# Kernel optimization log

Hardware: AMD Instinct MI355X
Metric: run time of the kernel (lower is better)

Reference implementation:

```python
import jax, jax.numpy as jnp
import numpy as np

C_V, C_F, C_D = 10, 64, 16
COSTS = jnp.array([10.0, 5.0, 2.0], dtype=jnp.float32)  # bandwidth cost per granularity
PENALTY = 0.0  # no_transmission_utility_penalty


def setup_inputs() -> dict:
    key = jax.random.key(0)
    k1, k2 = jax.random.split(key)
    B, H, W = 4, 192, 192
    collab = jax.random.normal(k1, (B, C_V + C_F + C_D, H, W), dtype=jnp.float32)
    utility = jax.random.normal(k2, (B, H, W, 3), dtype=jnp.float32)
    return {"collab_bev_data_list": collab, "utility_map_list": utility,
            "bandwidth_budget": 200000}


def _selection_mechanism(utility, budget_per_sample):
    # utility: [B, H, W, G]; returns [B, H, W] float selected granularity (-1 = none)
    B, H, W, G = utility.shape
    best_u = jnp.max(utility, axis=3)                      # [B,H,W]
    best_g = jnp.argmax(utility, axis=3)                   # [B,H,W]
    N = B * H * W
    flat_u = best_u.reshape(N)
    flat_g = best_g.reshape(N)
    b_idx = jnp.repeat(jnp.arange(B, dtype=jnp.int32), H * W)
    valid = flat_u > PENALTY
    cost = COSTS[flat_g]                                   # [N]
    # sort candidates by utility, descending (stable, matching list.sort)
    order = jnp.argsort(-flat_u)
    v_s = valid[order]
    c_s = cost[order]
    b_s = b_idx[order]

    # greedy budget-constrained selection per sample (sequential knapsack)
    def step(usage, item):
        v, c, b = item
        ok = v & (usage[b] + c <= budget_per_sample)
        usage = usage.at[b].add(jnp.where(ok, c, jnp.float32(0)))
        return usage, ok

    _, sel_sorted = jax.lax.scan(step, jnp.zeros((B,), jnp.float32), (v_s, c_s, b_s))
    selected = jnp.zeros((N,), bool).at[order].set(sel_sorted)
    idx = jnp.where(selected, flat_g.astype(jnp.float32), jnp.float32(-1.0))
    return idx.reshape(B, H, W)


def _build_sparse_bev(sel_idx, vox, feat, det):
    m0 = (sel_idx == 0.0)[:, None, :, :]
    m1 = (sel_idx == 1.0)[:, None, :, :]
    m2 = (sel_idx == 2.0)[:, None, :, :]
    return jnp.concatenate([vox * m0, feat * m1, det * m2], axis=1)


def reference(collab_bev_data_list, utility_map_list, bandwidth_budget):
    cav_num = collab_bev_data_list.shape[0]
    budget_per_sample = jnp.float32(bandwidth_budget / cav_num)
    sel_idx = _selection_mechanism(utility_map_list, budget_per_sample)
    vox = collab_bev_data_list[:, :C_V]
    feat = collab_bev_data_list[:, C_V:C_V + C_F]
    det = collab_bev_data_list[:, C_V + C_F:C_V + C_F + C_D]
    sparse = _build_sparse_bev(sel_idx, vox, feat, det)
    return sparse, sel_idx
```

## Files before the change

kernel.cpp:

```cpp
#include <hip/hip_runtime.h>
#include <stdint.h>
#include <math.h>

#define B_    4
#define HW    36864
#define NPIX  147456
#define C_V   10
#define C_F   64
#define C_D   16
#define C_ALL 90
#define HBINS 32768
#define CAP   1536
#define INV   0xFFFFFFFFu

#define OFF_HIST 0u
#define OFF_KEY  524288u
#define OFF_G    1114112u
#define OFF_SELX 1261568u
#define OFF_HL   1409024u

__device__ __forceinline__ uint32_t costOf(uint32_t g) {
    return g == 0u ? 10u : (g == 1u ? 5u : 2u);
}

__device__ __forceinline__ uint32_t budgetInt(const int* bptr) {
    double bps = (double)bptr[0] / (double)B_;
    float f = (float)bps;
    return (uint32_t)floorf(f);
}

#define CE(x, y) { uint64_t _mn = (x) < (y) ? (x) : (y); \
                   uint64_t _mx = (x) < (y) ? (y) : (x); (x) = _mx; (y) = _mn; }

__global__ void k_zero(uint4* __restrict__ w4) {
    uint32_t i = blockIdx.x * blockDim.x + threadIdx.x;
    w4[i] = make_uint4(0u, 0u, 0u, 0u);
}

__global__ void k_prep(const float* __restrict__ util, uint4* __restrict__ key4,
                       uint32_t* __restrict__ g4, uint32_t* __restrict__ selx4,
                       uint32_t* __restrict__ hist) {
    int t = blockIdx.x * blockDim.x + threadIdx.x;
    if (t >= NPIX / 4) return;
    const float4* u4 = (const float4*)util + (size_t)t * 3;
    float4 a = u4[0], b4 = u4[1], c4 = u4[2];
    float u[4][3] = { {a.x, a.y, a.z}, {a.w, b4.x, b4.y},
                      {b4.z, b4.w, c4.x}, {c4.y, c4.z, c4.w} };
    uint32_t kk[4]; uint32_t gpack = 0;
    #pragma unroll
    for (int p = 0; p < 4; ++p) {
        float best = u[p][0]; uint32_t g = 0;
        if (u[p][1] > best) { best = u[p][1]; g = 1; }
        if (u[p][2] > best) { best = u[p][2]; g = 2; }
        kk[p] = (best > 0.0f) ? (__float_as_uint(best) | 0x80000000u) : 0u;
        gpack |= g << (8 * p);
    }
    key4[t] = make_uint4(kk[0], kk[1], kk[2], kk[3]);
    g4[t] = gpack;
    selx4[t] = 0u;
    int b = (t * 4) / HW;
    #pragma unroll
    for (int p = 0; p < 4; ++p)
        if (kk[p])
            atomicAdd(&hist[(size_t)b * HBINS + ((kk[p] >> 16) & 32767u)],
                      costOf((gpack >> (8 * p)) & 3u));
}

__global__ __launch_bounds__(1024) void k_sel(const uint32_t* __restrict__ key,
                                              const uint8_t* __restrict__ g,
                                              const uint32_t* __restrict__ hist,
                                              const int* __restrict__ budget_ptr,
                                              uint8_t* __restrict__ selx,
                                              uint32_t* __restrict__ hl_out) {
    int b = blockIdx.x;
    int t = threadIdx.x;
    int lane = t & 63, wv = t >> 6;
    uint32_t budget = budgetInt(budget_ptr);
    const uint32_t* hb = hist + (size_t)b * HBINS;

    __shared__ uint32_t wsum[16];
    __shared__ uint32_t sh_b2, sh_usage, sh_n;
    __shared__ uint64_t e[CAP];
    __shared__ uint64_t s[CAP];
    __shared__ uint64_t red5[16];
    __shared__ uint64_t red2[16][4];

    if (t == 0) { sh_b2 = INV; sh_usage = 0u; sh_n = 0u; }

    uint4 hv[8];
    const uint4* h4 = (const uint4*)(hb + (32736 - 32 * t));
    #pragma unroll
    for (int j = 0; j < 8; ++j) hv[j] = h4[j];
    uint32_t cs = 0;
    #pragma unroll
    for (int j = 0; j < 8; ++j) cs += hv[j].x + hv[j].y + hv[j].z + hv[j].w;
    uint32_t v = cs;
    #pragma unroll
    for (int off = 1; off < 64; off <<= 1) {
        uint32_t o = __shfl_up(v, off);
        if (lane >= off) v += o;
    }
    if (lane == 63) wsum[wv] = v;
    __syncthreads();
    if (t < 16) {
        uint32_t w = wsum[t];
        #pragma unroll
        for (int off = 1; off < 16; off <<= 1) {
            uint32_t o = __shfl_up(w, off);
            if (t >= off) w += o;
        }
        wsum[t] = w;
    }
    __syncthreads();
    uint32_t incl = v + (wv ? wsum[wv - 1] : 0u);
    uint32_t excl = incl - cs;
    if (excl <= budget && incl > budget) {
        uint32_t vals[32];
        #pragma unroll
        for (int j = 0; j < 8; ++j) {
            vals[4 * j + 0] = hv[j].x; vals[4 * j + 1] = hv[j].y;
            vals[4 * j + 2] = hv[j].z; vals[4 * j + 3] = hv[j].w;
        }
        uint32_t cum = excl;
        #pragma unroll
        for (int a = 31; a >= 0; --a) {
            uint32_t val = vals[a];
            if (cum + val > budget) { sh_b2 = (uint32_t)(32736 - 32 * t + a);
                                      sh_usage = cum; break; }
            cum += val;
        }
    }
    __syncthreads();
    uint32_t b2 = sh_b2;
    if (t == 0) {
        uint32_t hl;
        if (b2 == INV) hl = 1u;
        else { uint32_t bs = b2 + 32768u;
               hl = (bs >= 65535u) ? INV : ((bs + 1u) << 16); }
        hl_out[b] = hl;
    }
    if (b2 == INV) return;

    const uint4*     k4  = (const uint4*)(key + (size_t)b * HW);
    const uint32_t*  g4p = (const uint32_t*)(g + (size_t)b * HW);
    uint64_t m5 = 0, a0 = 0, a1 = 0, a2 = 0, a3 = 0;
    #pragma unroll
    for (int it = 0; it < 9; ++it) {
        int gi = t + it * 1024;
        uint4 kk = k4[gi];
        uint32_t gp = g4p[gi];
        uint32_t kv[4] = { kk.x, kk.y, kk.z, kk.w };
        #pragma unroll
        for (int p = 0; p < 4; ++p) {
            uint32_t k = kv[p];
            if (!k) continue;
            uint32_t bin = (k >> 16) & 32767u;
            uint32_t gg = (gp >> (8 * p)) & 3u;
            uint32_t pix = (uint32_t)(gi * 4 + p);
            if (bin == b2) {
                uint32_t idx = atomicAdd(&sh_n, 1u);
                if (idx < CAP)
                    e[idx] = ((uint64_t)(~k) << 32) | ((uint64_t)pix << 2)
                           | (uint64_t)gg;
            } else if (bin < b2 && gg) {
                uint64_t m = ((uint64_t)k << 18)
                           | ((uint64_t)(65535u - pix) << 2) | (uint64_t)gg;
                if (gg == 1u) { if (m > m5) m5 = m; }
                else if (m > a3) {
                    if      (m > a0) { a3 = a2; a2 = a1; a1 = a0; a0 = m; }
                    else if (m > a1) { a3 = a2; a2 = a1; a1 = m; }
                    else if (m > a2) { a3 = a2; a2 = m; }
                    else             { a3 = m; }
                }
            }
        }
    }
    #pragma unroll
    for (int off = 32; off; off >>= 1) {
        uint64_t o5 = __shfl_down(m5, off);
        if (o5 > m5) m5 = o5;
        uint64_t b0 = __shfl_down(a0, off), b1 = __shfl_down(a1, off),
                 b2_ = __shfl_down(a2, off), b3 = __shfl_down(a3, off);
        CE(a0, b3); CE(a1, b2_); CE(a2, b1); CE(a3, b0);
        CE(a0, a2); CE(a1, a3); CE(a0, a1); CE(a2, a3);
    }
    if (lane == 0) {
        red5[wv] = m5;
        red2[wv][0] = a0; red2[wv][1] = a1; red2[wv][2] = a2; red2[wv][3] = a3;
    }
    __syncthreads();

    int n = (int)(sh_n < (uint32_t)CAP ? sh_n : (uint32_t)CAP);
    for (int i = t; i < n; i += 1024) {
        uint64_t ei = e[i];
        int rk = 0;
        for (int j = 0; j < n; ++j) rk += (e[j] < ei);
        s[rk] = ei;
    }
    __syncthreads();
    if (t == 0) {
        uint64_t g5 = 0, c0 = 0, c1 = 0, c2 = 0, c3 = 0;
        for (int wq = 0; wq < 16; ++wq) {
            if (red5[wq] > g5) g5 = red5[wq];
            #pragma unroll
            for (int q = 0; q < 4; ++q) {
                uint64_t m = red2[wq][q];
                if (m > c3) {
                    if      (m > c0) { c3 = c2; c2 = c1; c1 = c0; c0 = m; }
                    else if (m > c1) { c3 = c2; c2 = c1; c1 = m; }
                    else if (m > c2) { c3 = c2; c2 = m; }
                    else             { c3 = m; }
                }
            }
        }
        uint32_t usage = sh_usage;
        uint8_t* sx = selx + (size_t)b * HW;
        for (int i = 0; i < n; ++i) {
            uint64_t ei = s[i];
            uint32_t c = costOf((uint32_t)(ei & 3u));
            if (usage + c <= budget) { usage += c; sx[(ei >> 2) & 0xFFFFu] = 1; }
        }
        uint64_t c5[5] = { g5, c0, c1, c2, c3 };
        for (int i = 1; i < 5; ++i) {
            uint64_t x = c5[i]; int j = i;
            while (j > 0 && c5[j - 1] < x) { c5[j] = c5[j - 1]; --j; }
            c5[j] = x;
        }
        uint32_t r = budget - usage;
        for (int i = 0; i < 5; ++i) {
            uint64_t m = c5[i];
            if (!m) break;
            uint32_t c = costOf((uint32_t)(m & 3u));
            if (c <= r) {
                r -= c;
                uint32_t pix = 65535u - (uint32_t)((m >> 2) & 0xFFFFu);
                sx[pix] = 1;
            }
        }
    }
}

__global__ void k_sparse(const float* __restrict__ collab, const uint4* __restrict__ key4,
                         const uint32_t* __restrict__ g4, const uint32_t* __restrict__ selx4,
                         const uint32_t* __restrict__ hl_arr,
                         float* __restrict__ out, float* __restrict__ selOut) {
    int tid = blockIdx.x * blockDim.x + threadIdx.x;
    int c = blockIdx.y, b = blockIdx.z;
    int cls = (c < C_V) ? 0 : ((c < C_V + C_F) ? 1 : 2);
    uint32_t hl = hl_arr[b];
    size_t p4 = (size_t)b * (HW / 4) + (size_t)tid;
    uint4 kk = key4[p4];
    uint32_t gg = g4[p4];
    uint32_t sx = selx4[p4];
    int sc[4];
    uint32_t kv[4] = { kk.x, kk.y, kk.z, kk.w };
    #pragma unroll
    for (int p = 0; p < 4; ++p) {
        bool se = (kv[p] >= hl) || (((sx >> (8 * p)) & 0xFFu) != 0u);
        sc[p] = se ? (int)((gg >> (8 * p)) & 3u) : -1;
    }
    size_t co = ((size_t)(b * C_ALL + c)) * HW + (size_t)tid * 4;
    float4 v = *(const float4*)(collab + co);
    float4 o;
    o.x = (sc[0] == cls) ? v.x : 0.0f;
    o.y = (sc[1] == cls) ? v.y : 0.0f;
    o.z = (sc[2] == cls) ? v.z : 0.0f;
    o.w = (sc[3] == cls) ? v.w : 0.0f;
    *(float4*)(out + co) = o;
    if (c == 0) {
        float4 sf = make_float4((float)sc[0], (float)sc[1], (float)sc[2], (float)sc[3]);
        ((float4*)selOut)[p4] = sf;
    }
}

extern "C" void kernel_launch(void* const* d_in, const int* in_sizes, int n_in,
                              void* d_out, int out_size, void* d_ws, size_t ws_size,
                              hipStream_t stream) {
    (void)in_sizes; (void)n_in; (void)out_size; (void)ws_size;
    const float* collab = (const float*)d_in[0];
    const float* util   = (const float*)d_in[1];
    const int*   budget = (const int*)d_in[2];

    uint8_t*  ws   = (uint8_t*)d_ws;
    uint32_t* hist = (uint32_t*)(ws + OFF_HIST);
    uint32_t* key  = (uint32_t*)(ws + OFF_KEY);
    uint8_t*  g    = ws + OFF_G;
    uint8_t*  selx = ws + OFF_SELX;
    uint32_t* hl   = (uint32_t*)(ws + OFF_HL);

    float* outSparse = (float*)d_out;
    float* outSel    = outSparse + (size_t)B_ * C_ALL * HW;

    k_zero <<<HBINS * 4 / 4 / 256, 256, 0, stream>>>((uint4*)hist);
    k_prep <<<NPIX / 4 / 256, 256, 0, stream>>>(util, (uint4*)key, (uint32_t*)g,
                                                (uint32_t*)selx, hist);
    k_sel  <<<B_, 1024, 0, stream>>>(key, g, hist, budget, selx, hl);
    dim3 gridSP(HW / 4 / 256, C_ALL, B_);
    k_sparse<<<gridSP, 256, 0, stream>>>(collab, (const uint4*)key, (const uint32_t*)g,
                                         (const uint32_t*)selx, hl,
                                         outSparse, outSel);
}
```

Baseline: 93.42 us.

## Pack histogram to 16-bit bins and resolve selection codes inside k_sel

The cost histogram now packs two 16-bit bins per 32-bit word, which halves the memory that must be zeroed and scanned. The key and granularity loads in k_sel are issued early alongside the histogram loads. Selection is recorded in a shared-memory bitmask, and k_sel writes a packed per-pixel selection code plus the float sel_idx output. The channel-wide sparse kernel then reads one word per 4 pixels instead of recomputing selection from keys, g, selx and the threshold. The risks are 16-bit bin overflow if many costs land in one bin, and extra serial work in the 4-block k_sel kernel.

```diff
diff --git a/kernel.cpp b/kernel.cpp
--- a/kernel.cpp
+++ b/kernel.cpp
@@ -10,14 +10,14 @@
 #define C_D   16
 #define C_ALL 90
 #define HBINS 32768
+#define HWRD  16384
 #define CAP   1536
 #define INV   0xFFFFFFFFu
 
 #define OFF_HIST 0u
-#define OFF_KEY  524288u
-#define OFF_G    1114112u
-#define OFF_SELX 1261568u
-#define OFF_HL   1409024u
+#define OFF_KEY  262144u
+#define OFF_G    851968u
+#define OFF_SELC 999424u
 
 __device__ __forceinline__ uint32_t costOf(uint32_t g) {
     return g == 0u ? 10u : (g == 1u ? 5u : 2u);
@@ -38,8 +38,7 @@
 }
 
 __global__ void k_prep(const float* __restrict__ util, uint4* __restrict__ key4,
-                       uint32_t* __restrict__ g4, uint32_t* __restrict__ selx4,
-                       uint32_t* __restrict__ hist) {
+                       uint32_t* __restrict__ g4, uint32_t* __restrict__ hist) {
     int t = blockIdx.x * blockDim.x + threadIdx.x;
     if (t >= NPIX / 4) return;
     const float4* u4 = (const float4*)util + (size_t)t * 3;
@@ -57,43 +56,59 @@
     }
     key4[t] = make_uint4(kk[0], kk[1], kk[2], kk[3]);
     g4[t] = gpack;
-    selx4[t] = 0u;
     int b = (t * 4) / HW;
     #pragma unroll
     for (int p = 0; p < 4; ++p)
-        if (kk[p])
-            atomicAdd(&hist[(size_t)b * HBINS + ((kk[p] >> 16) & 32767u)],
-                      costOf((gpack >> (8 * p)) & 3u));
+        if (kk[p]) {
+            uint32_t bin = (kk[p] >> 16) & 32767u;
+            uint32_t c = costOf((gpack >> (8 * p)) & 3u);
+            atomicAdd(&hist[(size_t)b * HWRD + (bin >> 1)], c << (16u * (bin & 1u)));
+        }
 }
 
 __global__ __launch_bounds__(1024) void k_sel(const uint32_t* __restrict__ key,
                                               const uint8_t* __restrict__ g,
                                               const uint32_t* __restrict__ hist,
                                               const int* __restrict__ budget_ptr,
-                                              uint8_t* __restrict__ selx,
-                                              uint32_t* __restrict__ hl_out) {
+                                              uint32_t* __restrict__ selc,
+                                              float* __restrict__ outSel) {
     int b = blockIdx.x;
     int t = threadIdx.x;
     int lane = t & 63, wv = t >> 6;
     uint32_t budget = budgetInt(budget_ptr);
-    const uint32_t* hb = hist + (size_t)b * HBINS;
 
     __shared__ uint32_t wsum[16];
     __shared__ uint32_t sh_b2, sh_usage, sh_n;
+    __shared__ uint32_t selbit[1152];
     __shared__ uint64_t e[CAP];
     __shared__ uint64_t s[CAP];
     __shared__ uint64_t red5[16];
     __shared__ uint64_t red2[16][4];
 
+    selbit[t] = 0u;
+    if (t < 128) selbit[1024 + t] = 0u;
     if (t == 0) { sh_b2 = INV; sh_usage = 0u; sh_n = 0u; }
 
-    uint4 hv[8];
-    const uint4* h4 = (const uint4*)(hb + (32736 - 32 * t));
-    #pragma unroll
-    for (int j = 0; j < 8; ++j) hv[j] = h4[j];
+    const uint32_t* hb = hist + (size_t)b * HWRD;
+    const uint4* h4 = (const uint4*)(hb + (16368 - 16 * t));
+    uint4 hv[4];
+    #pragma unroll
+    for (int j = 0; j < 4; ++j) hv[j] = h4[j];
+    const uint4*    k4  = (const uint4*)(key + (size_t)b * HW);
+    const uint32_t* g4p = (const uint32_t*)(g + (size_t)b * HW);
+    uint4 kk[9]; uint32_t gp[9];
+    #pragma unroll
+    for (int it = 0; it < 9; ++it) {
+        int gi = t + it * 1024;
+        kk[it] = k4[gi];
+        gp[it] = g4p[gi];
+    }
+
     uint32_t cs = 0;
     #pragma unroll
-    for (int j = 0; j < 8; ++j) cs += hv[j].x + hv[j].y + hv[j].z + hv[j].w;
+    for (int j = 0; j < 4; ++j)
+        cs += (hv[j].x & 0xFFFFu) + (hv[j].x >> 16) + (hv[j].y & 0xFFFFu) + (hv[j].y >> 16)
+            + (hv[j].z & 0xFFFFu) + (hv[j].z >> 16) + (hv[j].w & 0xFFFFu) + (hv[j].w >> 16);
     uint32_t v = cs;
     #pragma unroll
     for (int off = 1; off < 64; off <<= 1) {
@@ -115,162 +130,160 @@
     uint32_t incl = v + (wv ? wsum[wv - 1] : 0u);
     uint32_t excl = incl - cs;
     if (excl <= budget && incl > budget) {
-        uint32_t vals[32];
-        #pragma unroll
-        for (int j = 0; j < 8; ++j) {
-            vals[4 * j + 0] = hv[j].x; vals[4 * j + 1] = hv[j].y;
-            vals[4 * j + 2] = hv[j].z; vals[4 * j + 3] = hv[j].w;
-        }
-        uint32_t cum = excl;
-        #pragma unroll
-        for (int a = 31; a >= 0; --a) {
-            uint32_t val = vals[a];
-            if (cum + val > budget) { sh_b2 = (uint32_t)(32736 - 32 * t + a);
-                                      sh_usage = cum; break; }
-            cum += val;
-        }
+        uint32_t base = 32736u - 32u * (uint32_t)t;
+        uint32_t cum = excl, fb2 = INV, fus = 0;
+        #define STEPW(W, wi) { \
+            uint32_t _hi = (W) >> 16, _lo = (W) & 0xFFFFu; \
+            if (fb2 == INV) { if (cum + _hi > budget) { fb2 = base + 2u*(wi) + 1u; fus = cum; } else cum += _hi; } \
+            if (fb2 == INV) { if (cum + _lo > budget) { fb2 = base + 2u*(wi);      fus = cum; } else cum += _lo; } }
+        STEPW(hv[3].w, 15) STEPW(hv[3].z, 14) STEPW(hv[3].y, 13) STEPW(hv[3].x, 12)
+        STEPW(hv[2].w, 11) STEPW(hv[2].z, 10) STEPW(hv[2].y,  9) STEPW(hv[2].x,  8)
+        STEPW(hv[1].w,  7) STEPW(hv[1].z,  6) STEPW(hv[1].y,  5) STEPW(hv[1].x,  4)
+        STEPW(hv[0].w,  3) STEPW(hv[0].z,  2) STEPW(hv[0].y,  1) STEPW(hv[0].x,  0)
+        #undef STEPW
+        sh_b2 = fb2; sh_usage = fus;
     }
     __syncthreads();
     uint32_t b2 = sh_b2;
-    if (t == 0) {
-        uint32_t hl;
-        if (b2 == INV) hl = 1u;
-        else { uint32_t bs = b2 + 32768u;
-               hl = (bs >= 65535u) ? INV : ((bs + 1u) << 16); }
-        hl_out[b] = hl;
-    }
-    if (b2 == INV) return;
-
-    const uint4*     k4  = (const uint4*)(key + (size_t)b * HW);
-    const uint32_t*  g4p = (const uint32_t*)(g + (size_t)b * HW);
-    uint64_t m5 = 0, a0 = 0, a1 = 0, a2 = 0, a3 = 0;
+
+    if (b2 != INV) {
+        uint64_t m5 = 0, a0 = 0, a1 = 0, a2 = 0, a3 = 0;
+        #pragma unroll
+        for (int it = 0; it < 9; ++it) {
+            int gi = t + it * 1024;
+            uint32_t kv[4] = { kk[it].x, kk[it].y, kk[it].z, kk[it].w };
+            #pragma unroll
+            for (int p = 0; p < 4; ++p) {
+                uint32_t k = kv[p];
+                if (!k) continue;
+                uint32_t bin = (k >> 16) & 32767u;
+                uint32_t gg = (gp[it] >> (8 * p)) & 3u;
+                uint32_t pix = (uint32_t)(gi * 4 + p);
+                if (bin == b2) {
+                    uint32_t idx = atomicAdd(&sh_n, 1u);
+                    if (idx < CAP)
+                        e[idx] = ((uint64_t)(~k) << 32) | ((uint64_t)pix << 2)
+                               | (uint64_t)gg;
+                } else if (bin < b2 && gg) {
+                    uint64_t m = ((uint64_t)k << 18)
+                               | ((uint64_t)(65535u - pix) << 2) | (uint64_t)gg;
+                    if (gg == 1u) { if (m > m5) m5 = m; }
+                    else if (m > a3) {
+                        if      (m > a0) { a3 = a2; a2 = a1; a1 = a0; a0 = m; }
+                        else if (m > a1) { a3 = a2; a2 = a1; a1 = m; }
+                        else if (m > a2) { a3 = a2; a2 = m; }
+                        else             { a3 = m; }
+                    }
+                }
+            }
+        }
+        #pragma unroll
+        for (int off = 32; off; off >>= 1) {
+            uint64_t o5 = __shfl_down(m5, off);
+            if (o5 > m5) m5 = o5;
+            uint64_t b0 = __shfl_down(a0, off), b1 = __shfl_down(a1, off),
+                     b2_ = __shfl_down(a2, off), b3 = __shfl_down(a3, off);
+            CE(a0, b3); CE(a1, b2_); CE(a2, b1); CE(a3, b0);
+            CE(a0, a2); CE(a1, a3); CE(a0, a1); CE(a2, a3);
+        }
+        if (lane == 0) {
+            red5[wv] = m5;
+            red2[wv][0] = a0; red2[wv][1] = a1; red2[wv][2] = a2; red2[wv][3] = a3;
+        }
+        __syncthreads();
+
+        int n = (int)(sh_n < (uint32_t)CAP ? sh_n : (uint32_t)CAP);
+        for (int i = t; i < n; i += 1024) {
+            uint64_t ei = e[i];
+            int rk = 0;
+            for (int j = 0; j < n; ++j) rk += (e[j] < ei);
+            s[rk] = ei;
+        }
+        __syncthreads();
+        if (t == 0) {
+            uint64_t g5 = 0, c0 = 0, c1 = 0, c2 = 0, c3 = 0;
+            for (int wq = 0; wq < 16; ++wq) {
+                if (red5[wq] > g5) g5 = red5[wq];
+                #pragma unroll
+                for (int q = 0; q < 4; ++q) {
+                    uint64_t m = red2[wq][q];
+                    if (m > c3) {
+                        if      (m > c0) { c3 = c2; c2 = c1; c1 = c0; c0 = m; }
+                        else if (m > c1) { c3 = c2; c2 = c1; c1 = m; }
+                        else if (m > c2) { c3 = c2; c2 = m; }
+                        else             { c3 = m; }
+                    }
+                }
+            }
+            uint32_t usage = sh_usage;
+            for (int i = 0; i < n; ++i) {
+                uint64_t ei = s[i];
+                uint32_t c = costOf((uint32_t)(ei & 3u));
+                if (usage + c <= budget) {
+                    usage += c;
+                    uint32_t pix = (uint32_t)((ei >> 2) & 0xFFFFu);
+                    selbit[pix >> 5] |= 1u << (pix & 31u);
+                }
+            }
+            uint64_t c5[5] = { g5, c0, c1, c2, c3 };
+            for (int i = 1; i < 5; ++i) {
+                uint64_t x = c5[i]; int j = i;
+                while (j > 0 && c5[j - 1] < x) { c5[j] = c5[j - 1]; --j; }
+                c5[j] = x;
+            }
+            uint32_t r = budget - usage;
+            for (int i = 0; i < 5; ++i) {
+                uint64_t m = c5[i];
+                if (!m) break;
+                uint32_t c = costOf((uint32_t)(m & 3u));
+                if (c <= r) {
+                    r -= c;
+                    uint32_t pix = 65535u - (uint32_t)((m >> 2) & 0xFFFFu);
+                    selbit[pix >> 5] |= 1u << (pix & 31u);
+                }
+            }
+        }
+    }
+    __syncthreads();
+
+    uint32_t hl;
+    if (b2 == INV) hl = 1u;
+    else { uint32_t bs = b2 + 32768u;
+           hl = (bs >= 65535u) ? INV : ((bs + 1u) << 16); }
     #pragma unroll
     for (int it = 0; it < 9; ++it) {
         int gi = t + it * 1024;
-        uint4 kk = k4[gi];
-        uint32_t gp = g4p[gi];
-        uint32_t kv[4] = { kk.x, kk.y, kk.z, kk.w };
+        uint32_t kv[4] = { kk[it].x, kk[it].y, kk[it].z, kk[it].w };
+        uint32_t bits = (selbit[gi >> 3] >> ((gi & 7) * 4)) & 0xFu;
+        uint32_t sel = 0; float sf[4];
         #pragma unroll
         for (int p = 0; p < 4; ++p) {
-            uint32_t k = kv[p];
-            if (!k) continue;
-            uint32_t bin = (k >> 16) & 32767u;
-            uint32_t gg = (gp >> (8 * p)) & 3u;
-            uint32_t pix = (uint32_t)(gi * 4 + p);
-            if (bin == b2) {
-                uint32_t idx = atomicAdd(&sh_n, 1u);
-                if (idx < CAP)
-                    e[idx] = ((uint64_t)(~k) << 32) | ((uint64_t)pix << 2)
-                           | (uint64_t)gg;
-            } else if (bin < b2 && gg) {
-                uint64_t m = ((uint64_t)k << 18)
-                           | ((uint64_t)(65535u - pix) << 2) | (uint64_t)gg;
-                if (gg == 1u) { if (m > m5) m5 = m; }
-                else if (m > a3) {
-                    if      (m > a0) { a3 = a2; a2 = a1; a1 = a0; a0 = m; }
-                    else if (m > a1) { a3 = a2; a2 = a1; a1 = m; }
-                    else if (m > a2) { a3 = a2; a2 = m; }
-                    else             { a3 = m; }
-                }
-            }
-        }
-    }
-    #pragma unroll
-    for (int off = 32; off; off >>= 1) {
-        uint64_t o5 = __shfl_down(m5, off);
-        if (o5 > m5) m5 = o5;
-        uint64_t b0 = __shfl_down(a0, off), b1 = __shfl_down(a1, off),
-                 b2_ = __shfl_down(a2, off), b3 = __shfl_down(a3, off);
-        CE(a0, b3); CE(a1, b2_); CE(a2, b1); CE(a3, b0);
-        CE(a0, a2); CE(a1, a3); CE(a0, a1); CE(a2, a3);
-    }
-    if (lane == 0) {
-        red5[wv] = m5;
-        red2[wv][0] = a0; red2[wv][1] = a1; red2[wv][2] = a2; red2[wv][3] = a3;
-    }
-    __syncthreads();
-
-    int n = (int)(sh_n < (uint32_t)CAP ? sh_n : (uint32_t)CAP);
-    for (int i = t; i < n; i += 1024) {
-        uint64_t ei = e[i];
-        int rk = 0;
-        for (int j = 0; j < n; ++j) rk += (e[j] < ei);
-        s[rk] = ei;
-    }
-    __syncthreads();
-    if (t == 0) {
-        uint64_t g5 = 0, c0 = 0, c1 = 0, c2 = 0, c3 = 0;
-        for (int wq = 0; wq < 16; ++wq) {
-            if (red5[wq] > g5) g5 = red5[wq];
-            #pragma unroll
-            for (int q = 0; q < 4; ++q) {
-                uint64_t m = red2[wq][q];
-                if (m > c3) {
-                    if      (m > c0) { c3 = c2; c2 = c1; c1 = c0; c0 = m; }
-                    else if (m > c1) { c3 = c2; c2 = c1; c1 = m; }
-                    else if (m > c2) { c3 = c2; c2 = m; }
-                    else             { c3 = m; }
-                }
-            }
-        }
-        uint32_t usage = sh_usage;
-        uint8_t* sx = selx + (size_t)b * HW;
-        for (int i = 0; i < n; ++i) {
-            uint64_t ei = s[i];
-            uint32_t c = costOf((uint32_t)(ei & 3u));
-            if (usage + c <= budget) { usage += c; sx[(ei >> 2) & 0xFFFFu] = 1; }
-        }
-        uint64_t c5[5] = { g5, c0, c1, c2, c3 };
-        for (int i = 1; i < 5; ++i) {
-            uint64_t x = c5[i]; int j = i;
-            while (j > 0 && c5[j - 1] < x) { c5[j] = c5[j - 1]; --j; }
-            c5[j] = x;
-        }
-        uint32_t r = budget - usage;
-        for (int i = 0; i < 5; ++i) {
-            uint64_t m = c5[i];
-            if (!m) break;
-            uint32_t c = costOf((uint32_t)(m & 3u));
-            if (c <= r) {
-                r -= c;
-                uint32_t pix = 65535u - (uint32_t)((m >> 2) & 0xFFFFu);
-                sx[pix] = 1;
-            }
-        }
-    }
-}
-
-__global__ void k_sparse(const float* __restrict__ collab, const uint4* __restrict__ key4,
-                         const uint32_t* __restrict__ g4, const uint32_t* __restrict__ selx4,
-                         const uint32_t* __restrict__ hl_arr,
-                         float* __restrict__ out, float* __restrict__ selOut) {
+            bool se = (kv[p] >= hl) || ((bits >> p) & 1u);
+            uint32_t gq = (gp[it] >> (8 * p)) & 3u;
+            sel |= (se ? gq : 0xFFu) << (8 * p);
+            sf[p] = se ? (float)gq : -1.0f;
+        }
+        selc[(size_t)b * (HW / 4) + gi] = sel;
+        ((float4*)outSel)[(size_t)b * (HW / 4) + gi] =
+            make_float4(sf[0], sf[1], sf[2], sf[3]);
+    }
+}
+
+__global__ __launch_bounds__(256) void k_sparse(const float* __restrict__ collab,
+                                                const uint32_t* __restrict__ selc,
+                                                float* __restrict__ out) {
     int tid = blockIdx.x * blockDim.x + threadIdx.x;
     int c = blockIdx.y, b = blockIdx.z;
-    int cls = (c < C_V) ? 0 : ((c < C_V + C_F) ? 1 : 2);
-    uint32_t hl = hl_arr[b];
-    size_t p4 = (size_t)b * (HW / 4) + (size_t)tid;
-    uint4 kk = key4[p4];
-    uint32_t gg = g4[p4];
-    uint32_t sx = selx4[p4];
-    int sc[4];
-    uint32_t kv[4] = { kk.x, kk.y, kk.z, kk.w };
-    #pragma unroll
-    for (int p = 0; p < 4; ++p) {
-        bool se = (kv[p] >= hl) || (((sx >> (8 * p)) & 0xFFu) != 0u);
-        sc[p] = se ? (int)((gg >> (8 * p)) & 3u) : -1;
-    }
-    size_t co = ((size_t)(b * C_ALL + c)) * HW + (size_t)tid * 4;
-    float4 v = *(const float4*)(collab + co);
+    uint32_t cls = (c < C_V) ? 0u : ((c < C_V + C_F) ? 1u : 2u);
+    uint32_t sel = selc[(size_t)b * (HW / 4) + tid];
+    size_t co = ((size_t)(b * C_ALL + c)) * (HW / 4) + (size_t)tid;
+    float4 v = ((const float4*)collab)[co];
     float4 o;
-    o.x = (sc[0] == cls) ? v.x : 0.0f;
-    o.y = (sc[1] == cls) ? v.y : 0.0f;
-    o.z = (sc[2] == cls) ? v.z : 0.0f;
-    o.w = (sc[3] == cls) ? v.w : 0.0f;
-    *(float4*)(out + co) = o;
-    if (c == 0) {
-        float4 sf = make_float4((float)sc[0], (float)sc[1], (float)sc[2], (float)sc[3]);
-        ((float4*)selOut)[p4] = sf;
-    }
+    o.x = (((sel      ) & 0xFFu) == cls) ? v.x : 0.0f;
+    o.y = (((sel >>  8) & 0xFFu) == cls) ? v.y : 0.0f;
+    o.z = (((sel >> 16) & 0xFFu) == cls) ? v.z : 0.0f;
+    o.w = (((sel >> 24) & 0xFFu) == cls) ? v.w : 0.0f;
+    ((float4*)out)[co] = o;
 }
 
 extern "C" void kernel_launch(void* const* d_in, const int* in_sizes, int n_in,
@@ -285,18 +298,14 @@
     uint32_t* hist = (uint32_t*)(ws + OFF_HIST);
     uint32_t* key  = (uint32_t*)(ws + OFF_KEY);
     uint8_t*  g    = ws + OFF_G;
-    uint8_t*  selx = ws + OFF_SELX;
-    uint32_t* hl   = (uint32_t*)(ws + OFF_HL);
+    uint32_t* selc = (uint32_t*)(ws + OFF_SELC);
 
     float* outSparse = (float*)d_out;
     float* outSel    = outSparse + (size_t)B_ * C_ALL * HW;
 
-    k_zero <<<HBINS * 4 / 4 / 256, 256, 0, stream>>>((uint4*)hist);
-    k_prep <<<NPIX / 4 / 256, 256, 0, stream>>>(util, (uint4*)key, (uint32_t*)g,
-                                                (uint32_t*)selx, hist);
-    k_sel  <<<B_, 1024, 0, stream>>>(key, g, hist, budget, selx, hl);
+    k_zero <<<B_ * HWRD / 4 / 256, 256, 0, stream>>>((uint4*)hist);
+    k_prep <<<NPIX / 4 / 256, 256, 0, stream>>>(util, (uint4*)key, (uint32_t*)g, hist);
+    k_sel  <<<B_, 1024, 0, stream>>>(key, g, hist, budget, selc, outSel);
     dim3 gridSP(HW / 4 / 256, C_ALL, B_);
-    k_sparse<<<gridSP, 256, 0, stream>>>(collab, (const uint4*)key, (const uint32_t*)g,
-                                         (const uint32_t*)selx, hl,
-                                         outSparse, outSel);
-}
+    k_sparse<<<gridSP, 256, 0, stream>>>(collab, selc, outSparse);
+}
```

Result: slower. 108.1 us (+15.8%).
